# Optimization experiments

Measured on AMD Instinct MI355X. Metric: run time of the kernel, lower is better.

The kernel has to match this reference:

```python
import jax, jax.numpy as jnp
import numpy as np

L_SEG = 20   # number of CFT segments (hard-coded in original forward)
M_CHEB = 8   # Chebyshev quadrature order per segment


def _cft_magnitude(x, modes):
    """|CFT(x)| at integer frequencies [0, modes).

    Faithful to vectorized_batched_cft_decomposed with L=20, M=8, but only
    evaluated at the first `modes` frequencies (identical values; the original
    computes all rfft freqs then slices). Segment loop is folded into a single
    einsum by absorbing the per-segment phase shift into the quadrature weights.
    x: (B, C, N) real. Returns (B, C, modes) float.
    """
    n = x.shape[-1]
    t = jnp.linspace(0.0, 1.0, n)
    freqs = jnp.arange(modes, dtype=x.dtype)  # rfftfreq(n, d=1/n)[:modes]
    seg_len = 1.0 / L_SEG
    starts = jnp.linspace(0.0, 1.0, L_SEG + 1)[:-1]  # (L,)
    k = jnp.arange(M_CHEB, dtype=x.dtype)
    cheb = -jnp.cos((2.0 * k + 1.0) * jnp.pi / (2.0 * M_CHEB))  # (M,) nodes in [-1,1]
    T = jnp.cos(k[:, None] * jnp.arccos(cheb)[None, :])  # (K=M, M) Chebyshev T_k at nodes
    angle = cheb[:, None] * (freqs[None, :] * (2.0 * jnp.pi * seg_len / 2.0))  # (M, F)
    Wr = jnp.einsum('km,mf->kf', T, jnp.cos(angle)) * (seg_len / 2.0)  # (M, F)
    Wi = jnp.einsum('km,mf->kf', T, -jnp.sin(angle)) * (seg_len / 2.0)
    # piecewise-linear interpolation of x at the Chebyshev nodes of every segment
    t_seg = starts[:, None] + seg_len / 2.0 * (cheb + 1.0)[None, :]  # (L, M)
    right = jnp.clip(jnp.searchsorted(t, t_seg), 0, n - 1)
    left = jnp.clip(right - 1, 0, None)
    t_l, t_r = t[left], t[right]
    denom = jnp.where(t_r - t_l == 0.0, 1.0, t_r - t_l)
    w_r = (t_seg - t_l) / denom
    w_l = 1.0 - w_r
    seg = w_l * x[:, :, left] + w_r * x[:, :, right]  # (B, C, L, M)
    # per-segment phase shift exp(-i*2*pi*f*a) folded into combined weights
    phi = 2.0 * jnp.pi * starts[:, None] * freqs[None, :]  # (L, F)
    cs, sn = jnp.cos(phi), jnp.sin(phi)
    Ar = Wr[None] * cs[:, None, :] + Wi[None] * sn[:, None, :]   # (L, M, F)
    Ai = -Wr[None] * sn[:, None, :] + Wi[None] * cs[:, None, :]
    real = jnp.einsum('bclm,lmf->bcf', seg, Ar)
    imag = jnp.einsum('bclm,lmf->bcf', seg, Ai)
    return jnp.sqrt(real * real + imag * imag)


def setup_inputs() -> dict:
    key = jax.random.key(0)
    ks = jax.random.split(key, 4)
    B, Cin, Cout, N, modes = 32, 64, 64, 8192, 32
    scale = 1.0 / (Cin * Cout)
    return {
        'x': jax.random.normal(ks[0], (B, Cin, N), dtype=jnp.float32),
        'w1_real': scale * jax.random.uniform(ks[1], (Cin, Cout, modes), dtype=jnp.float32),
        'w1_imag': scale * jax.random.uniform(ks[2], (Cin, Cout, modes), dtype=jnp.float32),
        'gate_w': jax.random.normal(ks[3], (Cout, Cin), dtype=jnp.float32) / np.sqrt(Cin),
        'ln_gamma': jnp.ones((modes,), dtype=jnp.float32),
        'ln_beta': jnp.zeros((modes,), dtype=jnp.float32),
    }


def reference(x, w1_real, w1_imag, gate_w, ln_gamma, ln_beta):
    n = x.shape[-1]
    n_rfft = n // 2 + 1
    modes = w1_real.shape[-1]
    x_fft = jnp.fft.rfft(x)  # (B, C, n_rfft) complex64
    # CFT magnitude is detached in the original (x_cft.detach())
    mag = jax.lax.stop_gradient(_cft_magnitude(x, modes))  # (B, C, modes)
    # LayerNorm over the modes axis (eps = 1e-5, torch default)
    mu = jnp.mean(mag, axis=-1, keepdims=True)
    var = jnp.mean((mag - mu) ** 2, axis=-1, keepdims=True)
    g_norm = (mag - mu) / jnp.sqrt(var + 1e-5) * ln_gamma + ln_beta
    # 1x1 conv (no bias) over channels, then sigmoid gate
    gate = jax.nn.sigmoid(jnp.einsum('oi,bif->bof', gate_w, g_norm))  # (B, Cout, modes)
    gated = x_fft[:, :, :modes] * gate  # requires Cin == Cout
    w1 = w1_real + 1j * w1_imag  # (Cin, Cout, modes) complex
    out_modes = jnp.einsum('bix,iox->box', gated, w1)
    pad = jnp.zeros(out_modes.shape[:2] + (n_rfft - modes,), dtype=out_modes.dtype)
    out_ft = jnp.concatenate([out_modes, pad], axis=-1)
    return jnp.fft.irfft(out_ft, n=n)
```

## Files before the change

kernel.cpp:

```cpp
#include <hip/hip_runtime.h>
#include <hip/hip_bf16.h>
#include <math.h>

#define NN    8192
#define NH    4096
#define NROWS 2048
#define FF    32
#define LM    160

static constexpr int TRIG   = 0;
static constexpr int W1RT   = 524288;
static constexpr int W1IT   = 655360;
static constexpr int GWT    = 786432;
static constexpr int AR_    = 790528;
static constexpr int AI_    = 795648;
static constexpr int WL_    = 800768;
static constexpr int WR_    = 800928;
static constexpr int IL_    = 801088;
static constexpr int IR_    = 801248;
static constexpr int XR_    = 801408;
static constexpr int XI_    = 866944;
static constexpr int GN_    = 932480;
static constexpr int ARAI   = 998016;
static constexpr int TRIGT_ = 1129088;

#define PI_D 3.14159265358979323846

__global__ __launch_bounds__(256) void k_setup(const float* __restrict__ w1r,
                                               const float* __restrict__ w1i,
                                               const float* __restrict__ gw,
                                               float* __restrict__ ws) {
  const int bid = blockIdx.x, tid = threadIdx.x;

  if (bid < 1024) {
    int idx = bid * 256 + tid;
    int k4 = idx >> 8, f = (idx >> 2) & 63, e = idx & 3;
    int n = 4 * k4 + e;
    int fr = f & 31;
    int p = (fr * n) & (NN - 1);
    float ang = (float)p * (float)(2.0 * PI_D / (double)NN);
    float s, c;
    sincosf(ang, &s, &c);
    float v = (f < 32) ? c : s;
    ws[TRIG + idx] = v;
    ws[TRIGT_ + f * NH + n] = v;
    return;
  }

  if (bid < 1044) {
    int t2 = (bid - 1024) * 256 + tid;
    if (t2 >= LM * FF) return;
    int j = t2 >> 5, f = t2 & 31;
    int l = j >> 3, m = j & 7;
    const double cheb[8] = {
      -0.98078528040323044913, -0.83146961230254523708,
      -0.55557023301960222474, -0.19509032201612826785,
       0.19509032201612826785,  0.55557023301960222474,
       0.83146961230254523708,  0.98078528040323044913 };

    double Wr = 0.0, Wi = 0.0;
    #pragma unroll
    for (int mm = 0; mm < 8; ++mm) {
      double c = cheb[mm];
      double T;
      if (m == 0) T = 1.0;
      else {
        double a = 1.0, b = c;
        for (int q = 1; q < m; ++q) { double t = 2.0 * c * b - a; a = b; b = t; }
        T = b;
      }
      double ang = c * (double)f * (PI_D * 0.05);
      Wr += T * cos(ang);
      Wi += T * (-sin(ang));
    }
    Wr *= 0.025; Wi *= 0.025;
    double phi = 2.0 * PI_D * ((double)l * 0.05) * (double)f;
    double cs = cos(phi), sn = sin(phi);
    ws[AR_ + j * FF + f] = (float)(Wr * cs + Wi * sn);
    ws[AI_ + j * FF + f] = (float)(-Wr * sn + Wi * cs);

    if (f == 0) {
      double v = (double)l * 0.05 + 0.025 * (cheb[m] + 1.0);
      int r = (int)(v * 8191.0);
      while ((double)r / 8191.0 < v) ++r;
      while (r > 0 && (double)(r - 1) / 8191.0 >= v) --r;
      if (r > 8191) r = 8191;
      int le = r - 1; if (le < 0) le = 0;
      double tl = (double)le / 8191.0, tr = (double)r / 8191.0;
      double den = (tr - tl == 0.0) ? 1.0 : (tr - tl);
      double wr = (v - tl) / den;
      ws[WL_ + j] = (float)(1.0 - wr);
      ws[WR_ + j] = (float)wr;
      ((int*)ws)[IL_ + j] = le;
      ((int*)ws)[IR_ + j] = r;
    }
    return;
  }

  {
    int idx = (bid - 1044) * 256 + tid;
    if (idx >= 32 * 64 * 64) return;
    int o = idx & 63, i = (idx >> 6) & 63, f = idx >> 12;
    ws[W1RT + (f * 64 + i) * 64 + o] = w1r[(i * 64 + o) * FF + f];
    ws[W1IT + (f * 64 + i) * 64 + o] = w1i[(i * 64 + o) * FF + f];
    if (idx < 4096) {
      ws[GWT + idx] = gw[(idx & 63) * 64 + (idx >> 6)];
    }
  }
}

__global__ __launch_bounds__(256) void k_fwd(const float* __restrict__ x,
                                             float* __restrict__ ws,
                                             float* __restrict__ part,
                                             const float* __restrict__ gamma,
                                             const float* __restrict__ beta) {
  __shared__ __align__(16) float smem[4096 + 16 + 4096];
  const int bid = blockIdx.x;
  const int t = threadIdx.x;

  if (bid < 2048) {
    const int rt = bid >> 6, jc = bid & 63;
    const int w = t >> 6, lane = t & 63;
    const int half = lane >> 5, fl = lane & 31;
    const int rblock = rt * 64;
    const int jb = jc * 64;

    #pragma unroll
    for (int p = 0; p < 4; ++p) {
      int idx = 256 * p + t;
      int row = idx >> 4, c4 = idx & 15;
      const float* __restrict__ xp = x + (size_t)(rblock + row) * NN + jb + c4 * 4;
      float4 a = *(const float4*)xp;
      float4 b = *(const float4*)(xp + NH);
      float4 u = make_float4(a.x + b.x, a.y + b.y, a.z + b.z, a.w + b.w);
      float4 v = make_float4(a.x - b.x, a.y - b.y, a.z - b.z, a.w - b.w);
      *(float4*)(&smem[row * 64 + c4 * 4]) = u;
      *(float4*)(&smem[4112 + row * 64 + c4 * 4]) = v;
    }

    float accC[8], accS[8];
    #pragma unroll
    for (int r = 0; r < 8; ++r) { accC[r] = 0.f; accS[r] = 0.f; }

    __syncthreads();

    const float* __restrict__ xb = &smem[(fl & 1) * 4112 + (w * 16 + half * 8) * 64];
    const float4* __restrict__ tg4 = (const float4*)(ws + TRIG);
    const size_t gb = (size_t)(jc * 16) * 64;

#define FWD_STEP(IT, TC, TS)                                                    \
    {                                                                           \
      _Pragma("unroll")                                                         \
      for (int j = 0; j < 8; ++j) {                                             \
        float4 xv = *(const float4*)(xb + j * 64 + (IT) * 4);                   \
        accC[j] = fmaf(xv.w, (TC).w, fmaf(xv.z, (TC).z,                         \
                  fmaf(xv.y, (TC).y, fmaf(xv.x, (TC).x, accC[j]))));            \
        accS[j] = fmaf(xv.w, (TS).w, fmaf(xv.z, (TS).z,                         \
                  fmaf(xv.y, (TS).y, fmaf(xv.x, (TS).x, accS[j]))));            \
      }                                                                         \
    }

    float4 tc = tg4[gb + fl];
    float4 tn = tg4[gb + 32 + fl];
    #pragma unroll 5
    for (int it = 0; it < 15; ++it) {
      float4 tc2 = tg4[gb + (size_t)(it + 1) * 64 + fl];
      float4 tn2 = tg4[gb + (size_t)(it + 1) * 64 + 32 + fl];
      FWD_STEP(it, tc, tn);
      tc = tc2; tn = tn2;
    }
    FWD_STEP(15, tc, tn);
#undef FWD_STEP

    float* __restrict__ pp = part + ((size_t)jc * NROWS + rblock + w * 16 + half * 8) * 64;
    #pragma unroll
    for (int j = 0; j < 8; ++j) {
      pp[j * 64 + fl]      = accC[j];
      pp[j * 64 + 32 + fl] = accS[j];
    }
    return;
  }

  {
    const int cb = bid - 2048;
    const int sub = t >> 6, li = t & 63;
    const int row = cb * 4 + sub;
    const float* __restrict__ xr = x + (size_t)row * NN;
    float (*seg)[LM] = (float (*)[LM])smem;
    #pragma unroll
    for (int g = 0; g < 3; ++g) {
      int j = li + 64 * g;
      if (j < LM) {
        int il = ((const int*)ws)[IL_ + j];
        int ir = ((const int*)ws)[IR_ + j];
        seg[sub][j] = ws[WL_ + j] * xr[il] + ws[WR_ + j] * xr[ir];
      }
    }
    __syncthreads();
    if (li < FF) {
      float re = 0.f, im = 0.f;
      #pragma unroll 8
      for (int j = 0; j < LM; ++j) {
        float sv = seg[sub][j];
        re = fmaf(sv, ws[AR_ + j * FF + li], re);
        im = fmaf(sv, ws[AI_ + j * FF + li], im);
      }
      float mag = sqrtf(re * re + im * im);
      float mu = mag;
      mu += __shfl_xor(mu, 1);  mu += __shfl_xor(mu, 2);  mu += __shfl_xor(mu, 4);
      mu += __shfl_xor(mu, 8);  mu += __shfl_xor(mu, 16);
      mu *= (1.0f / 32.0f);
      float d = mag - mu;
      float vv = d * d;
      vv += __shfl_xor(vv, 1);  vv += __shfl_xor(vv, 2);  vv += __shfl_xor(vv, 4);
      vv += __shfl_xor(vv, 8);  vv += __shfl_xor(vv, 16);
      vv *= (1.0f / 32.0f);
      float g = d / sqrtf(vv + 1e-5f) * gamma[li] + beta[li];
      ws[GN_ + row * FF + li] = g;
    }
  }
}

__global__ __launch_bounds__(256) void k_fred(const float* __restrict__ part,
                                              float* __restrict__ ws) {
  int idx = blockIdx.x * 256 + threadIdx.x;
  int row = idx >> 4, fq = idx & 15;
  const float4* __restrict__ p4 = (const float4*)part;
  float4 s = make_float4(0.f, 0.f, 0.f, 0.f);
  #pragma unroll 16
  for (int kc = 0; kc < 64; ++kc) {
    float4 v = p4[((size_t)kc * NROWS + row) * 16 + fq];
    s.x += v.x; s.y += v.y; s.z += v.z; s.w += v.w;
  }
  if (fq < 8) {
    *(float4*)(ws + XR_ + row * FF + fq * 4) = s;
  } else {
    float4 n = make_float4(-s.x, -s.y, -s.z, -s.w);
    *(float4*)(ws + XI_ + row * FF + (fq - 8) * 4) = n;
  }
}

__global__ __launch_bounds__(64) void k_gate(float* __restrict__ ws) {
  int bidx = blockIdx.x;
  int b = bidx >> 5, f = bidx & 31;
  int o = threadIdx.x;
  __shared__ float gn[64], gr[64], gi[64];
  int rowb = b * 64;
  gn[o] = ws[GN_ + (rowb + o) * FF + f];
  float xre = ws[XR_ + (rowb + o) * FF + f];
  float xim = ws[XI_ + (rowb + o) * FF + f];
  __syncthreads();
  float acc = 0.f;
  #pragma unroll 16
  for (int i = 0; i < 64; ++i)
    acc = fmaf(ws[GWT + i * 64 + o], gn[i], acc);
  float gate = 1.0f / (1.0f + expf(-acc));
  gr[o] = xre * gate;
  gi[o] = xim * gate;
  __syncthreads();
  float Yr = 0.f, Yi = 0.f;
  const float* __restrict__ w1rt = ws + W1RT + f * 4096;
  const float* __restrict__ w1it = ws + W1IT + f * 4096;
  #pragma unroll 8
  for (int i = 0; i < 64; ++i) {
    float a = gr[i], bb2 = gi[i];
    float wr = w1rt[i * 64 + o], wi = w1it[i * 64 + o];
    Yr = fmaf(a, wr, Yr); Yr = fmaf(-bb2, wi, Yr);
    Yi = fmaf(a, wi, Yi); Yi = fmaf(bb2, wr, Yi);
  }
  float* A = ws + ARAI + (size_t)(rowb + o) * 64;
  if (f == 0) {
    A[0]  = Yr * (1.0f / (float)NN);
    A[32] = 0.0f;
  } else {
    A[f]      = Yr * (2.0f / (float)NN);
    A[32 + f] = -Yi * (2.0f / (float)NN);
  }
}

__global__ __launch_bounds__(256) void k_inv(const float* __restrict__ ws,
                                             float* __restrict__ out) {
  __shared__ __align__(16) float As[32 * 64];
  const int blk = blockIdx.x;
  const int bb = blk >> 4, cc = blk & 15;
  const int t = threadIdx.x;
  const int w = t >> 6, lane = t & 63;
  const int rowbase = bb * 32;
  const float* __restrict__ trigt = ws + TRIGT_;
  const int colb = cc * 256 + lane * 4;

  float4 tg0 = *(const float4*)(trigt + (size_t)0 * NH + colb);
  float4 tg1 = *(const float4*)(trigt + (size_t)1 * NH + colb);
  float4 tg2 = *(const float4*)(trigt + (size_t)2 * NH + colb);
  float4 tg3 = *(const float4*)(trigt + (size_t)3 * NH + colb);

  #pragma unroll
  for (int p = 0; p < 2; ++p) {
    int idx = t + 256 * p;
    int r = idx >> 4, q = idx & 15;
    *(float4*)(&As[r * 64 + q * 4]) =
        *(const float4*)(ws + ARAI + (size_t)(rowbase + r) * 64 + q * 4);
  }

  float4 accE[8], accO[8];
  #pragma unroll
  for (int r = 0; r < 8; ++r) {
    accE[r] = make_float4(0.f, 0.f, 0.f, 0.f);
    accO[r] = make_float4(0.f, 0.f, 0.f, 0.f);
  }

  __syncthreads();

#define INV_STEP(F0)                                                            \
  {                                                                             \
    _Pragma("unroll")                                                           \
    for (int r = 0; r < 8; ++r) {                                               \
      float4 av = *(const float4*)(&As[(w * 8 + r) * 64 + (F0)]);               \
      accE[r].x = fmaf(av.x, tg0.x, accE[r].x); accE[r].y = fmaf(av.x, tg0.y, accE[r].y); \
      accE[r].z = fmaf(av.x, tg0.z, accE[r].z); accE[r].w = fmaf(av.x, tg0.w, accE[r].w); \
      accO[r].x = fmaf(av.y, tg1.x, accO[r].x); accO[r].y = fmaf(av.y, tg1.y, accO[r].y); \
      accO[r].z = fmaf(av.y, tg1.z, accO[r].z); accO[r].w = fmaf(av.y, tg1.w, accO[r].w); \
      accE[r].x = fmaf(av.z, tg2.x, accE[r].x); accE[r].y = fmaf(av.z, tg2.y, accE[r].y); \
      accE[r].z = fmaf(av.z, tg2.z, accE[r].z); accE[r].w = fmaf(av.z, tg2.w, accE[r].w); \
      accO[r].x = fmaf(av.w, tg3.x, accO[r].x); accO[r].y = fmaf(av.w, tg3.y, accO[r].y); \
      accO[r].z = fmaf(av.w, tg3.z, accO[r].z); accO[r].w = fmaf(av.w, tg3.w, accO[r].w); \
    }                                                                           \
  }

  for (int fo = 0; fo < 15; ++fo) {
    int f0 = fo * 4;
    float4 n0 = *(const float4*)(trigt + (size_t)(f0 + 4) * NH + colb);
    float4 n1 = *(const float4*)(trigt + (size_t)(f0 + 5) * NH + colb);
    float4 n2 = *(const float4*)(trigt + (size_t)(f0 + 6) * NH + colb);
    float4 n3 = *(const float4*)(trigt + (size_t)(f0 + 7) * NH + colb);
    INV_STEP(f0);
    tg0 = n0; tg1 = n1; tg2 = n2; tg3 = n3;
  }
  INV_STEP(60);
#undef INV_STEP

  #pragma unroll
  for (int r = 0; r < 8; ++r) {
    int row = rowbase + w * 8 + r;
    float4 E = accE[r], O = accO[r];
    float4 s0 = make_float4(E.x + O.x, E.y + O.y, E.z + O.z, E.w + O.w);
    float4 s1 = make_float4(E.x - O.x, E.y - O.y, E.z - O.z, E.w - O.w);
    *(float4*)(out + (size_t)row * NN + colb)      = s0;
    *(float4*)(out + (size_t)row * NN + colb + NH) = s1;
  }
}

extern "C" void kernel_launch(void* const* d_in, const int* in_sizes, int n_in,
                              void* d_out, int out_size, void* d_ws, size_t ws_size,
                              hipStream_t stream) {
  const float* x     = (const float*)d_in[0];
  const float* w1r   = (const float*)d_in[1];
  const float* w1i   = (const float*)d_in[2];
  const float* gw    = (const float*)d_in[3];
  const float* gamma = (const float*)d_in[4];
  const float* beta  = (const float*)d_in[5];
  float* out = (float*)d_out;
  float* ws = (float*)d_ws;
  float* part = (float*)d_out;

  hipLaunchKernelGGL(k_setup, dim3(1556), dim3(256), 0, stream, w1r, w1i, gw, ws);
  hipLaunchKernelGGL(k_fwd,   dim3(2560), dim3(256), 0, stream, x, ws, part, gamma, beta);
  hipLaunchKernelGGL(k_fred,  dim3(128),  dim3(256), 0, stream, part, ws);
  hipLaunchKernelGGL(k_gate,  dim3(1024), dim3(64),  0, stream, ws);
  hipLaunchKernelGGL(k_inv,   dim3(1024), dim3(256), 0, stream, ws, out);
}
```

Before: 178.3 us.

## Double-stage forward DFT tiles, stage twiddles in LDS, fuse partial reduction into gate

Result: no change. 178.0 us (-0.2%).

```diff
diff --git a/kernel.cpp b/kernel.cpp
--- a/kernel.cpp
+++ b/kernel.cpp
@@ -18,8 +18,6 @@
 static constexpr int WR_    = 800928;
 static constexpr int IL_    = 801088;
 static constexpr int IR_    = 801248;
-static constexpr int XR_    = 801408;
-static constexpr int XI_    = 866944;
 static constexpr int GN_    = 932480;
 static constexpr int ARAI   = 998016;
 static constexpr int TRIGT_ = 1129088;
@@ -109,80 +107,103 @@
   }
 }
 
-__global__ __launch_bounds__(256) void k_fwd(const float* __restrict__ x,
-                                             float* __restrict__ ws,
-                                             float* __restrict__ part,
-                                             const float* __restrict__ gamma,
-                                             const float* __restrict__ beta) {
-  __shared__ __align__(16) float smem[4096 + 16 + 4096];
+__global__ __launch_bounds__(256, 3) void k_fwd(const float* __restrict__ x,
+                                                float* __restrict__ ws,
+                                                float* __restrict__ part,
+                                                const float* __restrict__ gamma,
+                                                const float* __restrict__ beta) {
+  __shared__ __align__(16) float smem[8208 + 4096];
   const int bid = blockIdx.x;
   const int t = threadIdx.x;
 
-  if (bid < 2048) {
-    const int rt = bid >> 6, jc = bid & 63;
+  if (bid < 1024) {
+    const int rt_ = bid >> 5, jg = bid & 31;
     const int w = t >> 6, lane = t & 63;
     const int half = lane >> 5, fl = lane & 31;
-    const int rblock = rt * 64;
-    const int jb = jc * 64;
-
-    #pragma unroll
-    for (int p = 0; p < 4; ++p) {
-      int idx = 256 * p + t;
-      int row = idx >> 4, c4 = idx & 15;
-      const float* __restrict__ xp = x + (size_t)(rblock + row) * NN + jb + c4 * 4;
-      float4 a = *(const float4*)xp;
-      float4 b = *(const float4*)(xp + NH);
-      float4 u = make_float4(a.x + b.x, a.y + b.y, a.z + b.z, a.w + b.w);
-      float4 v = make_float4(a.x - b.x, a.y - b.y, a.z - b.z, a.w - b.w);
-      *(float4*)(&smem[row * 64 + c4 * 4]) = u;
-      *(float4*)(&smem[4112 + row * 64 + c4 * 4]) = v;
-    }
-
+    const int rblock = rt_ * 64;
+    const int jb0 = jg * 128;
+    float* __restrict__ tbuf = smem + 8208;
+    const float4* __restrict__ tg4src = (const float4*)(ws + TRIG) + (size_t)jg * 2048;
+
+    float4 ra[4], rb[4], rt4[4];
     float accC[8], accS[8];
     #pragma unroll
     for (int r = 0; r < 8; ++r) { accC[r] = 0.f; accS[r] = 0.f; }
 
-    __syncthreads();
-
-    const float* __restrict__ xb = &smem[(fl & 1) * 4112 + (w * 16 + half * 8) * 64];
-    const float4* __restrict__ tg4 = (const float4*)(ws + TRIG);
-    const size_t gb = (size_t)(jc * 16) * 64;
-
-#define FWD_STEP(IT, TC, TS)                                                    \
+#define STAGE_LOAD(JB, C)                                                       \
     {                                                                           \
       _Pragma("unroll")                                                         \
-      for (int j = 0; j < 8; ++j) {                                             \
-        float4 xv = *(const float4*)(xb + j * 64 + (IT) * 4);                   \
-        accC[j] = fmaf(xv.w, (TC).w, fmaf(xv.z, (TC).z,                         \
-                  fmaf(xv.y, (TC).y, fmaf(xv.x, (TC).x, accC[j]))));            \
-        accS[j] = fmaf(xv.w, (TS).w, fmaf(xv.z, (TS).z,                         \
-                  fmaf(xv.y, (TS).y, fmaf(xv.x, (TS).x, accS[j]))));            \
+      for (int p = 0; p < 4; ++p) {                                             \
+        int idx = 256 * p + t;                                                  \
+        int row = idx >> 4, cq = idx & 15;                                      \
+        const float* __restrict__ xp =                                          \
+            x + (size_t)(rblock + row) * NN + (JB) + cq * 4;                    \
+        ra[p] = *(const float4*)xp;                                             \
+        rb[p] = *(const float4*)(xp + NH);                                      \
+        rt4[p] = tg4src[(C) * 1024 + 256 * p + t];                              \
       }                                                                         \
     }
 
-    float4 tc = tg4[gb + fl];
-    float4 tn = tg4[gb + 32 + fl];
-    #pragma unroll 5
-    for (int it = 0; it < 15; ++it) {
-      float4 tc2 = tg4[gb + (size_t)(it + 1) * 64 + fl];
-      float4 tn2 = tg4[gb + (size_t)(it + 1) * 64 + 32 + fl];
-      FWD_STEP(it, tc, tn);
-      tc = tc2; tn = tn2;
-    }
-    FWD_STEP(15, tc, tn);
-#undef FWD_STEP
-
-    float* __restrict__ pp = part + ((size_t)jc * NROWS + rblock + w * 16 + half * 8) * 64;
-    #pragma unroll
-    for (int j = 0; j < 8; ++j) {
-      pp[j * 64 + fl]      = accC[j];
-      pp[j * 64 + 32 + fl] = accS[j];
-    }
+#define STAGE_WRITE()                                                           \
+    {                                                                           \
+      _Pragma("unroll")                                                         \
+      for (int p = 0; p < 4; ++p) {                                             \
+        int idx = 256 * p + t;                                                  \
+        int row = idx >> 4, cq = idx & 15;                                      \
+        float4 a = ra[p], b = rb[p];                                            \
+        *(float4*)(&smem[row * 64 + cq * 4]) =                                  \
+            make_float4(a.x + b.x, a.y + b.y, a.z + b.z, a.w + b.w);            \
+        *(float4*)(&smem[4112 + row * 64 + cq * 4]) =                           \
+            make_float4(a.x - b.x, a.y - b.y, a.z - b.z, a.w - b.w);            \
+        *(float4*)(&tbuf[(256 * p + t) * 4]) = rt4[p];                          \
+      }                                                                         \
+    }
+
+    const float* __restrict__ xb = &smem[(fl & 1) * 4112 + (w * 16 + half * 8) * 64];
+    const float* __restrict__ tb = &tbuf[fl * 4];
+
+#define COMPUTE()                                                               \
+    {                                                                           \
+      _Pragma("unroll 8")                                                       \
+      for (int it = 0; it < 16; ++it) {                                         \
+        float4 tc = *(const float4*)(tb + it * 256);                            \
+        float4 tn = *(const float4*)(tb + it * 256 + 128);                      \
+        _Pragma("unroll")                                                       \
+        for (int j = 0; j < 8; ++j) {                                           \
+          float4 xv = *(const float4*)(xb + j * 64 + it * 4);                   \
+          accC[j] = fmaf(xv.w, tc.w, fmaf(xv.z, tc.z,                           \
+                    fmaf(xv.y, tc.y, fmaf(xv.x, tc.x, accC[j]))));              \
+          accS[j] = fmaf(xv.w, tn.w, fmaf(xv.z, tn.z,                           \
+                    fmaf(xv.y, tn.y, fmaf(xv.x, tn.x, accS[j]))));              \
+        }                                                                       \
+      }                                                                         \
+    }
+
+    STAGE_LOAD(jb0, 0);
+    STAGE_WRITE();
+    __syncthreads();
+    STAGE_LOAD(jb0 + 64, 1);
+    COMPUTE();
+    __syncthreads();
+    STAGE_WRITE();
+    __syncthreads();
+    COMPUTE();
+
+#undef STAGE_LOAD
+#undef STAGE_WRITE
+#undef COMPUTE
+
+    float* __restrict__ pp = part + (size_t)jg * 131072 + (size_t)fl * 2048
+                                  + rblock + w * 16 + half * 8;
+    *(float4*)(pp)             = make_float4(accC[0], accC[1], accC[2], accC[3]);
+    *(float4*)(pp + 4)         = make_float4(accC[4], accC[5], accC[6], accC[7]);
+    *(float4*)(pp + 65536)     = make_float4(accS[0], accS[1], accS[2], accS[3]);
+    *(float4*)(pp + 65536 + 4) = make_float4(accS[4], accS[5], accS[6], accS[7]);
     return;
   }
 
   {
-    const int cb = bid - 2048;
+    const int cb = bid - 1024;
     const int sub = t >> 6, li = t & 63;
     const int row = cb * 4 + sub;
     const float* __restrict__ xr = x + (size_t)row * NN;
@@ -221,54 +242,45 @@
   }
 }
 
-__global__ __launch_bounds__(256) void k_fred(const float* __restrict__ part,
+__global__ __launch_bounds__(256) void k_gate(const float* __restrict__ part,
                                               float* __restrict__ ws) {
-  int idx = blockIdx.x * 256 + threadIdx.x;
-  int row = idx >> 4, fq = idx & 15;
-  const float4* __restrict__ p4 = (const float4*)part;
-  float4 s = make_float4(0.f, 0.f, 0.f, 0.f);
-  #pragma unroll 16
-  for (int kc = 0; kc < 64; ++kc) {
-    float4 v = p4[((size_t)kc * NROWS + row) * 16 + fq];
-    s.x += v.x; s.y += v.y; s.z += v.z; s.w += v.w;
-  }
-  if (fq < 8) {
-    *(float4*)(ws + XR_ + row * FF + fq * 4) = s;
-  } else {
-    float4 n = make_float4(-s.x, -s.y, -s.z, -s.w);
-    *(float4*)(ws + XI_ + row * FF + (fq - 8) * 4) = n;
-  }
-}
-
-__global__ __launch_bounds__(64) void k_gate(float* __restrict__ ws) {
-  int bidx = blockIdx.x;
-  int b = bidx >> 5, f = bidx & 31;
-  int o = threadIdx.x;
-  __shared__ float gn[64], gr[64], gi[64];
-  int rowb = b * 64;
-  gn[o] = ws[GN_ + (rowb + o) * FF + f];
-  float xre = ws[XR_ + (rowb + o) * FF + f];
-  float xim = ws[XI_ + (rowb + o) * FF + f];
+  const int bidx = blockIdx.x;
+  const int b = bidx >> 3, fg = bidx & 7;
+  const int sub = threadIdx.x >> 6, o = threadIdx.x & 63;
+  const int f = fg * 4 + sub;
+  __shared__ float gn[4][64], gr[4][64], gi[4][64];
+  const int rowb = b * 64;
+  const int row = rowb + o;
+
+  float sc = 0.f, ss = 0.f;
+  #pragma unroll 8
+  for (int jg = 0; jg < 32; ++jg) {
+    sc += part[(size_t)jg * 131072 + (size_t)f * 2048 + row];
+    ss += part[(size_t)jg * 131072 + (size_t)(32 + f) * 2048 + row];
+  }
+  float xre = sc, xim = -ss;
+
+  gn[sub][o] = ws[GN_ + row * FF + f];
   __syncthreads();
   float acc = 0.f;
   #pragma unroll 16
   for (int i = 0; i < 64; ++i)
-    acc = fmaf(ws[GWT + i * 64 + o], gn[i], acc);
+    acc = fmaf(ws[GWT + i * 64 + o], gn[sub][i], acc);
   float gate = 1.0f / (1.0f + expf(-acc));
-  gr[o] = xre * gate;
-  gi[o] = xim * gate;
+  gr[sub][o] = xre * gate;
+  gi[sub][o] = xim * gate;
   __syncthreads();
   float Yr = 0.f, Yi = 0.f;
   const float* __restrict__ w1rt = ws + W1RT + f * 4096;
   const float* __restrict__ w1it = ws + W1IT + f * 4096;
   #pragma unroll 8
   for (int i = 0; i < 64; ++i) {
-    float a = gr[i], bb2 = gi[i];
+    float a = gr[sub][i], b2 = gi[sub][i];
     float wr = w1rt[i * 64 + o], wi = w1it[i * 64 + o];
-    Yr = fmaf(a, wr, Yr); Yr = fmaf(-bb2, wi, Yr);
-    Yi = fmaf(a, wi, Yi); Yi = fmaf(bb2, wr, Yi);
-  }
-  float* A = ws + ARAI + (size_t)(rowb + o) * 64;
+    Yr = fmaf(a, wr, Yr); Yr = fmaf(-b2, wi, Yr);
+    Yi = fmaf(a, wi, Yi); Yi = fmaf(b2, wr, Yi);
+  }
+  float* __restrict__ A = ws + ARAI + (size_t)row * 64;
   if (f == 0) {
     A[0]  = Yr * (1.0f / (float)NN);
     A[32] = 0.0f;
@@ -364,8 +376,7 @@
   float* part = (float*)d_out;
 
   hipLaunchKernelGGL(k_setup, dim3(1556), dim3(256), 0, stream, w1r, w1i, gw, ws);
-  hipLaunchKernelGGL(k_fwd,   dim3(2560), dim3(256), 0, stream, x, ws, part, gamma, beta);
-  hipLaunchKernelGGL(k_fred,  dim3(128),  dim3(256), 0, stream, part, ws);
-  hipLaunchKernelGGL(k_gate,  dim3(1024), dim3(64),  0, stream, ws);
+  hipLaunchKernelGGL(k_fwd,   dim3(1536), dim3(256), 0, stream, x, ws, part, gamma, beta);
+  hipLaunchKernelGGL(k_gate,  dim3(256),  dim3(256), 0, stream, part, ws);
   hipLaunchKernelGGL(k_inv,   dim3(1024), dim3(256), 0, stream, ws, out);
 }
```
